# Optimization experiments

Hardware: AMD Instinct MI355X
Metric: run time of the kernel (lower is better)

## Reference

```python
import jax, jax.numpy as jnp
import numpy as np

MASK_VALUE = 0.0
LEAKY_SLOPE = 0.2  # tf.keras 'leaky_relu' activation default negative_slope

B, T, F, H, OUT = 256, 512, 256, 1024, 64


def setup_inputs() -> dict:
    key = jax.random.key(0)
    ks = jax.random.split(key, 5)
    x = jax.random.normal(ks[0], (B, T, F), dtype=jnp.float32)
    W = jax.random.normal(ks[1], (F, 4 * H), dtype=jnp.float32) * 0.05
    U = jax.random.normal(ks[2], (H, 4 * H), dtype=jnp.float32) * 0.05
    b = jnp.zeros((4 * H,), dtype=jnp.float32)
    W1 = jax.random.normal(ks[3], (3 * H, H), dtype=jnp.float32) * 0.02
    b1 = jnp.zeros((H,), dtype=jnp.float32)
    W2 = jax.random.normal(ks[4], (H, OUT), dtype=jnp.float32) * 0.02
    b2 = jnp.zeros((OUT,), dtype=jnp.float32)
    return {"x": x, "W": W, "U": U, "b": b, "W1": W1, "b1": b1, "W2": W2, "b2": b2}


def _lstm_final_state(x, mask, W, U, b):
    """Masked LSTM (Keras gate order i,f,g,o); masked steps carry state through.
    Returns final (h, c), each [B, H]. Dropout layers are identity at inference."""
    h0 = jnp.zeros((x.shape[0], H), dtype=x.dtype)
    c0 = jnp.zeros((x.shape[0], H), dtype=x.dtype)
    # Precompute input projection for all timesteps in one big GEMM: [B,T,4H]
    xz = jnp.einsum('btf,fg->btg', x, W) + b

    def step(carry, inp):
        h, c = carry
        xz_t, m_t = inp  # [B,4H], [B]
        z = xz_t + h @ U
        i, f, g, o = jnp.split(z, 4, axis=-1)
        i = jax.nn.sigmoid(i)
        f = jax.nn.sigmoid(f)
        g = jnp.tanh(g)
        o = jax.nn.sigmoid(o)
        c_new = f * c + i * g
        h_new = o * jnp.tanh(c_new)
        m = m_t[:, None]
        h = jnp.where(m, h_new, h)
        c = jnp.where(m, c_new, c)
        return (h, c), None

    xs = (jnp.swapaxes(xz, 0, 1), jnp.swapaxes(mask, 0, 1))  # time-major
    (h, c), _ = jax.lax.scan(step, (h0, c0), xs)
    return h, c


def reference(x, W, U, b, W1, b1, W2, b2):
    mask = jnp.any(x != MASK_VALUE, axis=2)  # [B,T]
    h, c = _lstm_final_state(x, mask, W, U, b)
    # return_state=True with return_sequences=False -> (out, h, c), out == h
    feat = jnp.concatenate([h, h, c], axis=1)  # [B, 3H]
    y = jax.nn.leaky_relu(feat @ W1 + b1, negative_slope=LEAKY_SLOPE)
    return y @ W2 + b2
```

## Files before the change

### kernel.cpp

```cpp
#include <hip/hip_runtime.h>

#define Tt_ 512
#define Ff_ 256
#define Hh_ 1024

typedef unsigned short u16;
typedef unsigned long long u64;
typedef __attribute__((ext_vector_type(8))) short bf16x8;
typedef __attribute__((ext_vector_type(4))) float f32x4;
typedef __attribute__((ext_vector_type(2))) unsigned int u32x2;

#define MFMA(a, b, c) __builtin_amdgcn_mfma_f32_16x16x32_bf16(a, b, c, 0, 0, 0)

__device__ __forceinline__ float bf2f(u16 u){
  union { unsigned int i; float f; } v; v.i = ((unsigned int)u) << 16; return v.f;
}
__device__ __forceinline__ u16 f2bf(float f){
  union { float f; unsigned int i; } v; v.f = f;
  return (u16)((v.i + 0x7FFFu + ((v.i >> 16) & 1u)) >> 16);
}
__device__ __forceinline__ float sigm(float z){ return 1.0f / (1.0f + __expf(-z)); }
__device__ __forceinline__ float tanh_(float z){ return 1.0f - 2.0f / (__expf(2.0f * z) + 1.0f); }
__device__ __forceinline__ float getE(const void* p, size_t i, int isf32){
  return isf32 ? ((const float*)p)[i] : bf2f(((const u16*)p)[i]);
}

template<int SEL>
__device__ __forceinline__ float qb(float v, int lbase){
#if __has_builtin(__builtin_amdgcn_mov_dpp)
  int r = __builtin_amdgcn_mov_dpp(__builtin_bit_cast(int, v), SEL * 0x55, 0xF, 0xF, true);
  return __builtin_bit_cast(float, r);
#else
  return __shfl(v, lbase + SEL, 64);
#endif
}

__global__ void detect_dtype(const u16* __restrict__ p, int* __restrict__ flag){
  int tid = threadIdx.x;
  int plausible = 0;
  for (int i = tid; i < 4096; i += 256){
    u16 u = p[2 * i];
    int ex = (u >> 7) & 0xFF;
    plausible += (((u & 0x7FFF) == 0) || (ex >= 87 && ex <= 133)) ? 1 : 0;
  }
  __shared__ int red[256];
  red[tid] = plausible; __syncthreads();
  for (int s = 128; s > 0; s >>= 1){ if (tid < s) red[tid] += red[tid + s]; __syncthreads(); }
  if (tid == 0) *flag = (red[0] < (4096 * 3) / 5) ? 1 : 0;
}

__global__ void convert_x(const void* __restrict__ x, u16* __restrict__ xb, const int* __restrict__ flags){
  size_t i = ((size_t)blockIdx.x * 256 + threadIdx.x) * 8;
  if (flags[0]){
    const float* xf = (const float*)x + i;
    u16 o[8];
    #pragma unroll
    for (int j = 0; j < 8; ++j) o[j] = f2bf(xf[j]);
    *(bf16x8*)(xb + i) = *(const bf16x8*)o;
  } else {
    *(bf16x8*)(xb + i) = *(const bf16x8*)((const u16*)x + i);
  }
}

__global__ void pack_wu(const void* __restrict__ W, const void* __restrict__ U,
                        const int* __restrict__ flags, u16* __restrict__ WUp){
  int fW = flags[1], fU = flags[2];
  int u = blockIdx.x * 256 + threadIdx.x;
  int nt = u / 10240;
  int rem = u - nt * 10240;
  int kg = rem >> 6, c64 = rem & 63;
  int pc = nt * 64 + c64;
  int g = pc & 3;
  int gb = ((g & 1) << 1) | (g >> 1);
  int oc = gb * 1024 + (pc >> 2);
  u16* dst = WUp + (size_t)u * 8;
  #pragma unroll
  for (int j = 0; j < 8; ++j){
    int k = kg * 8 + j;
    float v = (k < 256) ? getE(W, (size_t)k * 4096 + oc, fW)
                        : getE(U, (size_t)(k - 256) * 4096 + oc, fU);
    dst[j] = f2bf(v);
  }
}

__global__ void pack_w1(const void* __restrict__ W1, const int* __restrict__ flags, u16* __restrict__ W1p){
  int f1 = flags[3];
  int u = blockIdx.x * 256 + threadIdx.x;
  int nt = u >> 14;
  int kg = (u >> 6) & 255, c64 = u & 63;
  int n = nt * 64 + c64;
  u16* dst = W1p + (size_t)u * 8;
  #pragma unroll
  for (int j = 0; j < 8; ++j){
    int k = kg * 8 + j;
    float a = (k < 1024) ? getE(W1, (size_t)k * 1024 + n, f1) : 0.0f;
    a += getE(W1, (size_t)(k + 1024) * 1024 + n, f1);
    dst[j] = f2bf(a);
  }
}

__global__ void pack_w2(const void* __restrict__ W2, const int* __restrict__ flags, u16* __restrict__ W2p){
  int f2 = flags[4];
  int u = blockIdx.x * 256 + threadIdx.x;
  int kg = u >> 6, c64 = u & 63;
  u16* dst = W2p + (size_t)u * 8;
  #pragma unroll
  for (int j = 0; j < 8; ++j) dst[j] = f2bf(getE(W2, (size_t)(kg * 8 + j) * 64 + c64, f2));
}

__global__ void pack_bias(const u16* __restrict__ b, float* __restrict__ br){
  int u = blockIdx.x * 256 + threadIdx.x;
  int g = u & 3;
  int gb = ((g & 1) << 1) | (g >> 1);
  br[u] = bf2f(b[gb * 1024 + (u >> 2)]);
}

__global__ void mask_kernel(const u16* __restrict__ xb, unsigned char* __restrict__ mkT){
  int w = threadIdx.x >> 6, lane = threadIdx.x & 63;
  int row = blockIdx.x * 4 + w;
  u32x2 v = *((const u32x2*)(xb + (size_t)row * 256) + lane);
  int nz = (((v.x & 0x7FFF7FFFu) | (v.y & 0x7FFF7FFFu)) != 0u);
  int a = __any(nz);
  if (lane == 0){
    int b = row >> 9, t = row & 511;
    mkT[(size_t)t * 256 + b] = (unsigned char)(a ? 1 : 0);
  }
}

__launch_bounds__(512, 1)
__global__ void lstm_step(const u16* __restrict__ x, const u16* __restrict__ WUp,
                          const float* __restrict__ br, const unsigned char* __restrict__ mkT,
                          u16* __restrict__ hb0, u16* __restrict__ hb1,
                          u16* __restrict__ cfin, unsigned int* bar){
  __shared__ u64 hsm[8192];
  __shared__ u16 hstg[1024];
  __shared__ u16 Bc[2][22528];
  const int tid = threadIdx.x, bid = blockIdx.x;
  const int lane = tid & 63, w = tid >> 6;
  const int quad = lane >> 4, l15 = lane & 15;
  const int g  = (bid >> 3) & 7;
  const int c  = (bid & 7) | ((bid >> 6) << 3);
  const int r0 = g * 32;
  const int tile = w >> 2;
  const int nt = c * 2 + tile;
  const int bc0 = (w & 3) * 16 + l15;
  const u16* Bb = WUp + (size_t)nt * 81920;
  const int pc0 = c * 128 + w * 16 + l15;
  const float bias0 = br[pc0];
  const int slot = lane & 3, lbase = lane & 60;
  const int jl0 = w * 4 + (l15 >> 2);
  const int rowE = quad * 4;
  const size_t xrowA = (size_t)(r0 + l15) * (Tt_ * Ff_);
  const size_t xrowB = xrowA + (size_t)16 * Tt_ * Ff_;
  const int swzA = (l15 & 7) << 4;
  char* hb = (char*)hsm;
  unsigned int* mybar = bar + (g << 5);
  const int hr   = tid >> 4;
  const int hc16 = tid & 15;
  const size_t hgoff = (size_t)(r0 + hr) * Hh_ + hc16 * 4;
  const int hldsb = hr * 2048;
  const int hswz = (hr & 7) << 4;
  const int hcb = hc16 * 8;

  for (int i = tid; i < 5632; i += 512){
    int tl = i / 2816, rem = i - tl * 2816;
    *(bf16x8*)&Bc[tl][rem * 8] =
      *(const bf16x8*)(WUp + (size_t)(c * 2 + tl) * 81920 + (size_t)rem * 8);
  }
  __syncthreads();

  f32x4 cst[2];
  { f32x4 z4 = {0.f, 0.f, 0.f, 0.f}; cst[0] = z4; cst[1] = z4; }

  f32x4 accx[2];
  { f32x4 i0 = {bias0, bias0, bias0, bias0}; accx[0] = i0; accx[1] = i0; }
  {
    const u16* xp = x;
    #pragma unroll
    for (int ks = 0; ks < 8; ++ks){
      int kq = ks * 32 + quad * 8;
      bf16x8 a0 = *(const bf16x8*)(xp + xrowA + kq);
      bf16x8 a1 = *(const bf16x8*)(xp + xrowB + kq);
      bf16x8 b0 = *(const bf16x8*)(&Bc[tile][ks * 2048 + quad * 512 + bc0 * 8]);
      accx[0] = MFMA(a0, b0, accx[0]);
      accx[1] = MFMA(a1, b0, accx[1]);
    }
  }

  for (int t = 0; t < Tt_; ++t){
    const u16* hin  = (t & 1) ? hb1 : hb0;
    u16*       hout = (t & 1) ? hb0 : hb1;

    u64 hA[8], hB[8];
    #pragma unroll
    for (int i = 0; i < 8; ++i)
      hA[i] = __hip_atomic_load((const u64*)(hin + hgoff + i * 64),
                                __ATOMIC_RELAXED, __HIP_MEMORY_SCOPE_AGENT);
    #pragma unroll
    for (int i = 0; i < 8; ++i)
      hB[i] = __hip_atomic_load((const u64*)(hin + hgoff + (i + 8) * 64),
                                __ATOMIC_RELAXED, __HIP_MEMORY_SCOPE_AGENT);

    unsigned int mka = *(const unsigned int*)(mkT + (size_t)t * 256 + r0 + rowE);
    unsigned int mkb = *(const unsigned int*)(mkT + (size_t)t * 256 + r0 + rowE + 16);

    f32x4 acc[2];
    acc[0] = accx[0]; acc[1] = accx[1];

    #pragma unroll
    for (int i = 0; i < 8; ++i)
      *(u64*)(hb + hldsb + ((i * 128 + hcb) ^ hswz)) = hA[i];
    __syncthreads();

    #pragma unroll
    for (int ks = 0; ks < 3; ++ks){
      int cb = ks * 64 + quad * 16;
      bf16x8 a0 = *(const bf16x8*)(hb + l15 * 2048 + (cb ^ swzA));
      bf16x8 a1 = *(const bf16x8*)(hb + (l15 + 16) * 2048 + (cb ^ swzA));
      bf16x8 b0 = *(const bf16x8*)(&Bc[tile][(ks + 8) * 2048 + quad * 512 + bc0 * 8]);
      acc[0] = MFMA(a0, b0, acc[0]);
      acc[1] = MFMA(a1, b0, acc[1]);
    }
    #pragma unroll
    for (int ks = 3; ks < 16; ++ks){
      int cb = ks * 64 + quad * 16;
      bf16x8 a0 = *(const bf16x8*)(hb + l15 * 2048 + (cb ^ swzA));
      bf16x8 a1 = *(const bf16x8*)(hb + (l15 + 16) * 2048 + (cb ^ swzA));
      bf16x8 b0 = *(const bf16x8*)(Bb + (size_t)((ks + 8) * 4 + quad) * 512 + bc0 * 8);
      acc[0] = MFMA(a0, b0, acc[0]);
      acc[1] = MFMA(a1, b0, acc[1]);
    }

    #pragma unroll
    for (int i = 0; i < 8; ++i)
      *(u64*)(hb + hldsb + (((i + 8) * 128 + hcb) ^ hswz)) = hB[i];
    __syncthreads();

    #pragma unroll
    for (int ks = 16; ks < 32; ++ks){
      int cb = ks * 64 + quad * 16;
      bf16x8 a0 = *(const bf16x8*)(hb + l15 * 2048 + (cb ^ swzA));
      bf16x8 a1 = *(const bf16x8*)(hb + (l15 + 16) * 2048 + (cb ^ swzA));
      bf16x8 b0 = *(const bf16x8*)(Bb + (size_t)((ks + 8) * 4 + quad) * 512 + bc0 * 8);
      acc[0] = MFMA(a0, b0, acc[0]);
      acc[1] = MFMA(a1, b0, acc[1]);
    }

    #pragma unroll
    for (int mf = 0; mf < 2; ++mf){
      unsigned int mk4 = mf ? mkb : mka;
      #pragma unroll
      for (int reg = 0; reg < 4; ++reg){
        float z = acc[mf][reg];
        float v = (slot == 1) ? tanh_(z) : sigm(z);
        float vi = qb<0>(v, lbase);
        float vg = qb<1>(v, lbase);
        float vf = qb<2>(v, lbase);
        float vo = qb<3>(v, lbase);
        float cv = cst[mf][reg];
        float cn = fmaf(vf, cv, vi * vg);
        float hn = vo * tanh_(cn);
        if (!((mk4 >> (8 * reg)) & 1u)){
          cn = cv;
          int rl = rowE + reg + mf * 16;
          int jh = c * 32 + jl0;
          hn = bf2f(*(const u16*)(hb + rl * 2048 + ((jh * 2) ^ ((rl & 7) << 4))));
        }
        cst[mf][reg] = cn;
        if (slot == 0){
          int rl = rowE + reg + mf * 16;
          hstg[rl * 32 + jl0] = f2bf(hn);
        }
      }
    }
    __syncthreads();

    if (tid < 256){
      u64 val = ((const u64*)hstg)[tid];
      __hip_atomic_store((u64*)(hout + (size_t)(r0 + (tid >> 3)) * Hh_ + c * 32 + (tid & 7) * 4),
                         val, __ATOMIC_RELAXED, __HIP_MEMORY_SCOPE_AGENT);
    }
    __syncthreads();

    if (t < Tt_ - 1){
      if (tid == 0)
        __hip_atomic_fetch_add(mybar, 1u, __ATOMIC_RELAXED, __HIP_MEMORY_SCOPE_AGENT);

      { f32x4 i0 = {bias0, bias0, bias0, bias0}; accx[0] = i0; accx[1] = i0; }
      {
        const u16* xp = x + (size_t)(t + 1) * Ff_;
        #pragma unroll
        for (int ks = 0; ks < 8; ++ks){
          int kq = ks * 32 + quad * 8;
          bf16x8 a0 = *(const bf16x8*)(xp + xrowA + kq);
          bf16x8 a1 = *(const bf16x8*)(xp + xrowB + kq);
          bf16x8 b0 = *(const bf16x8*)(&Bc[tile][ks * 2048 + quad * 512 + bc0 * 8]);
          accx[0] = MFMA(a0, b0, accx[0]);
          accx[1] = MFMA(a1, b0, accx[1]);
        }
      }

      if (tid == 0){
        const unsigned int target = (unsigned int)(t + 1) * 32u;
        while (__hip_atomic_load(mybar, __ATOMIC_RELAXED, __HIP_MEMORY_SCOPE_AGENT) < target)
          __builtin_amdgcn_s_sleep(1);
      }
      __syncthreads();
    }
  }

  #pragma unroll
  for (int mf = 0; mf < 2; ++mf)
    #pragma unroll
    for (int reg = 0; reg < 4; ++reg)
      if (slot == 0){
        int r = r0 + rowE + reg + mf * 16;
        cfin[(size_t)r * Hh_ + c * 32 + jl0] = f2bf(cst[mf][reg]);
      }
}

__launch_bounds__(256, 1)
__global__ void gemm_head(const u16* __restrict__ A1, const u16* __restrict__ A2,
                          int kSplit, int kSlices, const u16* __restrict__ Bp,
                          int Ntiles, const u16* __restrict__ bias, int act,
                          void* __restrict__ outp, int ldOut, int outF32){
  const int tid = threadIdx.x, bid = blockIdx.x;
  const int lane = tid & 63, w = tid >> 6;
  const int wm = w >> 1, wn = w & 1;
  const int quad = lane >> 4, l15 = lane & 15;
  const int mt = bid / Ntiles, nt = bid - mt * Ntiles;
  const int r0 = mt * 64 + wm * 32 + l15;
  const size_t arow0 = (size_t)r0 * 1024;
  const size_t arow1 = arow0 + (size_t)16 * 1024;
  const int bc0 = wn * 32 + l15;
  const u16* Bb = Bp + (size_t)nt * kSlices * 2048;
  f32x4 acc[2][2];
  { f32x4 z4 = {0.f, 0.f, 0.f, 0.f}; acc[0][0] = z4; acc[0][1] = z4; acc[1][0] = z4; acc[1][1] = z4; }
  #pragma unroll 4
  for (int ks = 0; ks < kSlices; ++ks){
    const u16* ap; int kq;
    if (ks < kSplit){ ap = A1; kq = ks * 32 + quad * 8; }
    else            { ap = A2; kq = (ks - kSplit) * 32 + quad * 8; }
    bf16x8 a0 = *(const bf16x8*)(ap + arow0 + kq);
    bf16x8 a1 = *(const bf16x8*)(ap + arow1 + kq);
    const u16* bp = Bb + (size_t)(ks * 4 + quad) * 512;
    bf16x8 b0 = *(const bf16x8*)(bp + bc0 * 8);
    bf16x8 b1 = *(const bf16x8*)(bp + bc0 * 8 + 128);
    acc[0][0] = MFMA(a0, b0, acc[0][0]);
    acc[0][1] = MFMA(a0, b1, acc[0][1]);
    acc[1][0] = MFMA(a1, b0, acc[1][0]);
    acc[1][1] = MFMA(a1, b1, acc[1][1]);
  }
  #pragma unroll
  for (int mf = 0; mf < 2; ++mf)
    #pragma unroll
    for (int nf = 0; nf < 2; ++nf){
      int cB = nt * 64 + bc0 + nf * 16;
      #pragma unroll
      for (int reg = 0; reg < 4; ++reg){
        int r = mt * 64 + wm * 32 + mf * 16 + quad * 4 + reg;
        float zv = acc[mf][nf][reg] + bf2f(bias[cB]);
        if (act) zv = (zv > 0.f) ? zv : 0.2f * zv;
        if (outF32) ((float*)outp)[(size_t)r * ldOut + cB] = zv;
        else        ((u16*)outp)[(size_t)r * ldOut + cB] = f2bf(zv);
      }
    }
}

extern "C" void kernel_launch(void* const* d_in, const int* in_sizes, int n_in,
                              void* d_out, int out_size, void* d_ws, size_t ws_size,
                              hipStream_t stream){
  const void* x  = d_in[0];
  const void* W  = d_in[1];
  const void* U  = d_in[2];
  const u16*  b  = (const u16*)d_in[3];
  const void* W1 = d_in[4];
  const u16*  b1 = (const u16*)d_in[5];
  const void* W2 = d_in[6];
  const u16*  b2 = (const u16*)d_in[7];
  char* ws = (char*)d_ws;
  size_t o = 0;
  u16* WUp = (u16*)(ws + o);            o += 10485760;
  u16* W1p = (u16*)(ws + o);            o += 4194304;
  u16* W2p = (u16*)(ws + o);            o += 131072;
  float* br = (float*)(ws + o);         o += 16384;
  unsigned char* mk = (unsigned char*)(ws + o); o += 131072;
  u16* hb0 = (u16*)(ws + o);            o += 524288;
  u16* hb1 = (u16*)(ws + o);            o += 524288;
  u16* cfin = (u16*)(ws + o);           o += 524288;
  u16* yb  = (u16*)(ws + o);            o += 524288;
  unsigned int* bar = (unsigned int*)(ws + o); o += 1024;
  int* flg = (int*)(ws + o);            o += 512;
  u16* xb  = (u16*)(ws + o);            o += 67108864;
  if (ws_size < o) return;

  hipMemsetAsync(hb0, 0, 524288, stream);
  hipMemsetAsync(bar, 0, 1024, stream);
  detect_dtype<<<1, 256, 0, stream>>>((const u16*)x,  flg + 0);
  detect_dtype<<<1, 256, 0, stream>>>((const u16*)W,  flg + 1);
  detect_dtype<<<1, 256, 0, stream>>>((const u16*)U,  flg + 2);
  detect_dtype<<<1, 256, 0, stream>>>((const u16*)W1, flg + 3);
  detect_dtype<<<1, 256, 0, stream>>>((const u16*)W2, flg + 4);
  convert_x<<<16384, 256, 0, stream>>>(x, xb, flg);
  pack_wu<<<2560, 256, 0, stream>>>(W, U, flg, WUp);
  pack_w1<<<1024, 256, 0, stream>>>(W1, flg, W1p);
  pack_w2<<<32, 256, 0, stream>>>(W2, flg, W2p);
  pack_bias<<<16, 256, 0, stream>>>(b, br);
  mask_kernel<<<32768, 256, 0, stream>>>(xb, mk);
  lstm_step<<<256, 512, 0, stream>>>(xb, WUp, br, mk, hb0, hb1, cfin, bar);
  gemm_head<<<64, 256, 0, stream>>>(hb0, cfin, 32, 64, W1p, 16, b1, 1, yb, 1024, 0);
  gemm_head<<<4, 256, 0, stream>>>(yb, yb, 32, 32, W2p, 1, b2, 0, d_out, 64, 1);
}
```

Baseline: 4.946 ms.

## Replace per-group atomic counter barrier with per-block step flags polled by all waves

```diff
diff --git a/kernel.cpp b/kernel.cpp
--- a/kernel.cpp
+++ b/kernel.cpp
@@ -131,7 +131,7 @@
 __global__ void lstm_step(const u16* __restrict__ x, const u16* __restrict__ WUp,
                           const float* __restrict__ br, const unsigned char* __restrict__ mkT,
                           u16* __restrict__ hb0, u16* __restrict__ hb1,
-                          u16* __restrict__ cfin, unsigned int* bar){
+                          u16* __restrict__ cfin, unsigned int* flg32){
   __shared__ u64 hsm[8192];
   __shared__ u16 hstg[1024];
   __shared__ u16 Bc[2][22528];
@@ -154,7 +154,9 @@
   const size_t xrowB = xrowA + (size_t)16 * Tt_ * Ff_;
   const int swzA = (l15 & 7) << 4;
   char* hb = (char*)hsm;
-  unsigned int* mybar = bar + (g << 5);
+  const unsigned int* fpA = flg32 + (((g << 5) + (lane & 15)) << 4);
+  const unsigned int* fpB = fpA + (16 << 4);
+  unsigned int* myflag = flg32 + (((g << 5) + c) << 4);
   const int hr   = tid >> 4;
   const int hc16 = tid & 15;
   const size_t hgoff = (size_t)(r0 + hr) * Hh_ + hc16 * 4;
@@ -190,12 +192,20 @@
   for (int t = 0; t < Tt_; ++t){
     const u16* hin  = (t & 1) ? hb1 : hb0;
     u16*       hout = (t & 1) ? hb0 : hb1;
-
+    const unsigned int tgt = (unsigned int)t;
+
+    while (__ballot(__hip_atomic_load(fpA, __ATOMIC_RELAXED, __HIP_MEMORY_SCOPE_AGENT) >= tgt)
+           != ~0ull){}
+    asm volatile("" ::: "memory");
     u64 hA[8], hB[8];
     #pragma unroll
     for (int i = 0; i < 8; ++i)
       hA[i] = __hip_atomic_load((const u64*)(hin + hgoff + i * 64),
                                 __ATOMIC_RELAXED, __HIP_MEMORY_SCOPE_AGENT);
+
+    while (__ballot(__hip_atomic_load(fpB, __ATOMIC_RELAXED, __HIP_MEMORY_SCOPE_AGENT) >= tgt)
+           != ~0ull){}
+    asm volatile("" ::: "memory");
     #pragma unroll
     for (int i = 0; i < 8; ++i)
       hB[i] = __hip_atomic_load((const u64*)(hin + hgoff + (i + 8) * 64),
@@ -282,30 +292,22 @@
     }
     __syncthreads();
 
+    if (tid == 0)
+      __hip_atomic_store(myflag, (unsigned int)(t + 1),
+                         __ATOMIC_RELAXED, __HIP_MEMORY_SCOPE_AGENT);
+
     if (t < Tt_ - 1){
-      if (tid == 0)
-        __hip_atomic_fetch_add(mybar, 1u, __ATOMIC_RELAXED, __HIP_MEMORY_SCOPE_AGENT);
-
       { f32x4 i0 = {bias0, bias0, bias0, bias0}; accx[0] = i0; accx[1] = i0; }
-      {
-        const u16* xp = x + (size_t)(t + 1) * Ff_;
-        #pragma unroll
-        for (int ks = 0; ks < 8; ++ks){
-          int kq = ks * 32 + quad * 8;
-          bf16x8 a0 = *(const bf16x8*)(xp + xrowA + kq);
-          bf16x8 a1 = *(const bf16x8*)(xp + xrowB + kq);
-          bf16x8 b0 = *(const bf16x8*)(&Bc[tile][ks * 2048 + quad * 512 + bc0 * 8]);
-          accx[0] = MFMA(a0, b0, accx[0]);
-          accx[1] = MFMA(a1, b0, accx[1]);
-        }
+      const u16* xp = x + (size_t)(t + 1) * Ff_;
+      #pragma unroll
+      for (int ks = 0; ks < 8; ++ks){
+        int kq = ks * 32 + quad * 8;
+        bf16x8 a0 = *(const bf16x8*)(xp + xrowA + kq);
+        bf16x8 a1 = *(const bf16x8*)(xp + xrowB + kq);
+        bf16x8 b0 = *(const bf16x8*)(&Bc[tile][ks * 2048 + quad * 512 + bc0 * 8]);
+        accx[0] = MFMA(a0, b0, accx[0]);
+        accx[1] = MFMA(a1, b0, accx[1]);
       }
-
-      if (tid == 0){
-        const unsigned int target = (unsigned int)(t + 1) * 32u;
-        while (__hip_atomic_load(mybar, __ATOMIC_RELAXED, __HIP_MEMORY_SCOPE_AGENT) < target)
-          __builtin_amdgcn_s_sleep(1);
-      }
-      __syncthreads();
     }
   }
 
@@ -389,13 +391,13 @@
   u16* hb1 = (u16*)(ws + o);            o += 524288;
   u16* cfin = (u16*)(ws + o);           o += 524288;
   u16* yb  = (u16*)(ws + o);            o += 524288;
-  unsigned int* bar = (unsigned int*)(ws + o); o += 1024;
+  unsigned int* flg32 = (unsigned int*)(ws + o); o += 16384;
   int* flg = (int*)(ws + o);            o += 512;
   u16* xb  = (u16*)(ws + o);            o += 67108864;
   if (ws_size < o) return;
 
   hipMemsetAsync(hb0, 0, 524288, stream);
-  hipMemsetAsync(bar, 0, 1024, stream);
+  hipMemsetAsync(flg32, 0, 16384, stream);
   detect_dtype<<<1, 256, 0, stream>>>((const u16*)x,  flg + 0);
   detect_dtype<<<1, 256, 0, stream>>>((const u16*)W,  flg + 1);
   detect_dtype<<<1, 256, 0, stream>>>((const u16*)U,  flg + 2);
@@ -407,7 +409,7 @@
   pack_w2<<<32, 256, 0, stream>>>(W2, flg, W2p);
   pack_bias<<<16, 256, 0, stream>>>(b, br);
   mask_kernel<<<32768, 256, 0, stream>>>(xb, mk);
-  lstm_step<<<256, 512, 0, stream>>>(xb, WUp, br, mk, hb0, hb1, cfin, bar);
+  lstm_step<<<256, 512, 0, stream>>>(xb, WUp, br, mk, hb0, hb1, cfin, flg32);
   gemm_head<<<64, 256, 0, stream>>>(hb0, cfin, 32, 64, W1p, 16, b1, 1, yb, 1024, 0);
   gemm_head<<<4, 256, 0, stream>>>(yb, yb, 32, 32, W2p, 1, b2, 0, d_out, 64, 1);
 }
```

Result: slower. 5.119 ms (+3.5%).

## Split LSTM step rows across 16 waves with 1024-thread blocks

Applied to the files above, without the earlier changes.

```diff
diff --git a/kernel.cpp b/kernel.cpp
--- a/kernel.cpp
+++ b/kernel.cpp
@@ -127,7 +127,7 @@
   }
 }
 
-__launch_bounds__(512, 1)
+__launch_bounds__(1024, 1)
 __global__ void lstm_step(const u16* __restrict__ x, const u16* __restrict__ WUp,
                           const float* __restrict__ br, const unsigned char* __restrict__ mkT,
                           u16* __restrict__ hb0, u16* __restrict__ hb1,
@@ -141,49 +141,45 @@
   const int g  = (bid >> 3) & 7;
   const int c  = (bid & 7) | ((bid >> 6) << 3);
   const int r0 = g * 32;
-  const int tile = w >> 2;
-  const int nt = c * 2 + tile;
-  const int bc0 = (w & 3) * 16 + l15;
-  const u16* Bb = WUp + (size_t)nt * 81920;
-  const int pc0 = c * 128 + w * 16 + l15;
+  const int rh = w & 1;
+  const int cs = w >> 1;
+  const int tile = cs >> 2;
+  const int bc0 = (cs & 3) * 16 + l15;
+  const u16* Bb = WUp + (size_t)(c * 2 + tile) * 81920;
+  const int pc0 = c * 128 + cs * 16 + l15;
   const float bias0 = br[pc0];
   const int slot = lane & 3, lbase = lane & 60;
-  const int jl0 = w * 4 + (l15 >> 2);
+  const int jl0 = cs * 4 + (l15 >> 2);
+  const int rowL = rh * 16;
   const int rowE = quad * 4;
-  const size_t xrowA = (size_t)(r0 + l15) * (Tt_ * Ff_);
-  const size_t xrowB = xrowA + (size_t)16 * Tt_ * Ff_;
+  const size_t xrow = (size_t)(r0 + rowL + l15) * (Tt_ * Ff_);
   const int swzA = (l15 & 7) << 4;
   char* hb = (char*)hsm;
   unsigned int* mybar = bar + (g << 5);
-  const int hr   = tid >> 4;
-  const int hc16 = tid & 15;
-  const size_t hgoff = (size_t)(r0 + hr) * Hh_ + hc16 * 4;
+  const int hr   = tid >> 5;
+  const int hc32 = tid & 31;
+  const size_t hgoff = (size_t)(r0 + hr) * Hh_ + hc32 * 4;
   const int hldsb = hr * 2048;
   const int hswz = (hr & 7) << 4;
-  const int hcb = hc16 * 8;
-
-  for (int i = tid; i < 5632; i += 512){
+  const int hcb = hc32 * 8;
+
+  for (int i = tid; i < 5632; i += 1024){
     int tl = i / 2816, rem = i - tl * 2816;
     *(bf16x8*)&Bc[tl][rem * 8] =
       *(const bf16x8*)(WUp + (size_t)(c * 2 + tl) * 81920 + (size_t)rem * 8);
   }
   __syncthreads();
 
-  f32x4 cst[2];
-  { f32x4 z4 = {0.f, 0.f, 0.f, 0.f}; cst[0] = z4; cst[1] = z4; }
-
-  f32x4 accx[2];
-  { f32x4 i0 = {bias0, bias0, bias0, bias0}; accx[0] = i0; accx[1] = i0; }
+  f32x4 cst = {0.f, 0.f, 0.f, 0.f};
+
+  f32x4 accx = {bias0, bias0, bias0, bias0};
   {
     const u16* xp = x;
     #pragma unroll
     for (int ks = 0; ks < 8; ++ks){
-      int kq = ks * 32 + quad * 8;
-      bf16x8 a0 = *(const bf16x8*)(xp + xrowA + kq);
-      bf16x8 a1 = *(const bf16x8*)(xp + xrowB + kq);
+      bf16x8 a0 = *(const bf16x8*)(xp + xrow + ks * 32 + quad * 8);
       bf16x8 b0 = *(const bf16x8*)(&Bc[tile][ks * 2048 + quad * 512 + bc0 * 8]);
-      accx[0] = MFMA(a0, b0, accx[0]);
-      accx[1] = MFMA(a1, b0, accx[1]);
+      accx = MFMA(a0, b0, accx);
     }
   }
 
@@ -191,86 +187,74 @@
     const u16* hin  = (t & 1) ? hb1 : hb0;
     u16*       hout = (t & 1) ? hb0 : hb1;
 
-    u64 hA[8], hB[8];
-    #pragma unroll
-    for (int i = 0; i < 8; ++i)
-      hA[i] = __hip_atomic_load((const u64*)(hin + hgoff + i * 64),
+    u64 hA[4], hB[4];
+    #pragma unroll
+    for (int i = 0; i < 4; ++i)
+      hA[i] = __hip_atomic_load((const u64*)(hin + hgoff + i * 128),
                                 __ATOMIC_RELAXED, __HIP_MEMORY_SCOPE_AGENT);
     #pragma unroll
-    for (int i = 0; i < 8; ++i)
-      hB[i] = __hip_atomic_load((const u64*)(hin + hgoff + (i + 8) * 64),
+    for (int i = 0; i < 4; ++i)
+      hB[i] = __hip_atomic_load((const u64*)(hin + hgoff + (i + 4) * 128),
                                 __ATOMIC_RELAXED, __HIP_MEMORY_SCOPE_AGENT);
 
-    unsigned int mka = *(const unsigned int*)(mkT + (size_t)t * 256 + r0 + rowE);
-    unsigned int mkb = *(const unsigned int*)(mkT + (size_t)t * 256 + r0 + rowE + 16);
-
-    f32x4 acc[2];
-    acc[0] = accx[0]; acc[1] = accx[1];
-
-    #pragma unroll
-    for (int i = 0; i < 8; ++i)
-      *(u64*)(hb + hldsb + ((i * 128 + hcb) ^ hswz)) = hA[i];
+    unsigned int mk4 = *(const unsigned int*)(mkT + (size_t)t * 256 + r0 + rowL + rowE);
+
+    f32x4 acc = accx;
+
+    #pragma unroll
+    for (int i = 0; i < 4; ++i)
+      *(u64*)(hb + hldsb + ((i * 256 + hcb) ^ hswz)) = hA[i];
     __syncthreads();
 
     #pragma unroll
     for (int ks = 0; ks < 3; ++ks){
       int cb = ks * 64 + quad * 16;
-      bf16x8 a0 = *(const bf16x8*)(hb + l15 * 2048 + (cb ^ swzA));
-      bf16x8 a1 = *(const bf16x8*)(hb + (l15 + 16) * 2048 + (cb ^ swzA));
+      bf16x8 a0 = *(const bf16x8*)(hb + (rowL + l15) * 2048 + (cb ^ swzA));
       bf16x8 b0 = *(const bf16x8*)(&Bc[tile][(ks + 8) * 2048 + quad * 512 + bc0 * 8]);
-      acc[0] = MFMA(a0, b0, acc[0]);
-      acc[1] = MFMA(a1, b0, acc[1]);
+      acc = MFMA(a0, b0, acc);
     }
     #pragma unroll
     for (int ks = 3; ks < 16; ++ks){
       int cb = ks * 64 + quad * 16;
-      bf16x8 a0 = *(const bf16x8*)(hb + l15 * 2048 + (cb ^ swzA));
-      bf16x8 a1 = *(const bf16x8*)(hb + (l15 + 16) * 2048 + (cb ^ swzA));
+      bf16x8 a0 = *(const bf16x8*)(hb + (rowL + l15) * 2048 + (cb ^ swzA));
       bf16x8 b0 = *(const bf16x8*)(Bb + (size_t)((ks + 8) * 4 + quad) * 512 + bc0 * 8);
-      acc[0] = MFMA(a0, b0, acc[0]);
-      acc[1] = MFMA(a1, b0, acc[1]);
-    }
-
-    #pragma unroll
-    for (int i = 0; i < 8; ++i)
-      *(u64*)(hb + hldsb + (((i + 8) * 128 + hcb) ^ hswz)) = hB[i];
+      acc = MFMA(a0, b0, acc);
+    }
+
+    #pragma unroll
+    for (int i = 0; i < 4; ++i)
+      *(u64*)(hb + hldsb + (((i + 4) * 256 + hcb) ^ hswz)) = hB[i];
     __syncthreads();
 
     #pragma unroll
     for (int ks = 16; ks < 32; ++ks){
       int cb = ks * 64 + quad * 16;
-      bf16x8 a0 = *(const bf16x8*)(hb + l15 * 2048 + (cb ^ swzA));
-      bf16x8 a1 = *(const bf16x8*)(hb + (l15 + 16) * 2048 + (cb ^ swzA));
+      bf16x8 a0 = *(const bf16x8*)(hb + (rowL + l15) * 2048 + (cb ^ swzA));
       bf16x8 b0 = *(const bf16x8*)(Bb + (size_t)((ks + 8) * 4 + quad) * 512 + bc0 * 8);
-      acc[0] = MFMA(a0, b0, acc[0]);
-      acc[1] = MFMA(a1, b0, acc[1]);
-    }
-
-    #pragma unroll
-    for (int mf = 0; mf < 2; ++mf){
-      unsigned int mk4 = mf ? mkb : mka;
-      #pragma unroll
-      for (int reg = 0; reg < 4; ++reg){
-        float z = acc[mf][reg];
-        float v = (slot == 1) ? tanh_(z) : sigm(z);
-        float vi = qb<0>(v, lbase);
-        float vg = qb<1>(v, lbase);
-        float vf = qb<2>(v, lbase);
-        float vo = qb<3>(v, lbase);
-        float cv = cst[mf][reg];
-        float cn = fmaf(vf, cv, vi * vg);
-        float hn = vo * tanh_(cn);
-        if (!((mk4 >> (8 * reg)) & 1u)){
-          cn = cv;
-          int rl = rowE + reg + mf * 16;
-          int jh = c * 32 + jl0;
-          hn = bf2f(*(const u16*)(hb + rl * 2048 + ((jh * 2) ^ ((rl & 7) << 4))));
-        }
-        cst[mf][reg] = cn;
-        if (slot == 0){
-          int rl = rowE + reg + mf * 16;
-          hstg[rl * 32 + jl0] = f2bf(hn);
-        }
+      acc = MFMA(a0, b0, acc);
+    }
+
+    #pragma unroll
+    for (int reg = 0; reg < 4; ++reg){
+      float z = acc[reg];
+      float v = (slot == 1) ? tanh_(z) : sigm(z);
+      float vi = qb<0>(v, lbase);
+      float vg = qb<1>(v, lbase);
+      float vf = qb<2>(v, lbase);
+      float vo = qb<3>(v, lbase);
+      float cv = cst[reg];
+      float cn = fmaf(vf, cv, vi * vg);
+      float hn = vo * tanh_(cn);
+      if (!((mk4 >> (8 * reg)) & 1u)){
+        cn = cv;
+        int rl = rowL + rowE + reg;
+        int jh = c * 32 + jl0;
+        hn = bf2f(*(const u16*)(hb + rl * 2048 + ((jh * 2) ^ ((rl & 7) << 4))));
+      }
+      cst[reg] = cn;
+      if (slot == 0){
+        int rl = rowL + rowE + reg;
+        hstg[rl * 32 + jl0] = f2bf(hn);
       }
     }
     __syncthreads();
@@ -286,17 +270,14 @@
       if (tid == 0)
         __hip_atomic_fetch_add(mybar, 1u, __ATOMIC_RELAXED, __HIP_MEMORY_SCOPE_AGENT);
 
-      { f32x4 i0 = {bias0, bias0, bias0, bias0}; accx[0] = i0; accx[1] = i0; }
+      accx = (f32x4){bias0, bias0, bias0, bias0};
       {
         const u16* xp = x + (size_t)(t + 1) * Ff_;
         #pragma unroll
         for (int ks = 0; ks < 8; ++ks){
-          int kq = ks * 32 + quad * 8;
-          bf16x8 a0 = *(const bf16x8*)(xp + xrowA + kq);
-          bf16x8 a1 = *(const bf16x8*)(xp + xrowB + kq);
+          bf16x8 a0 = *(const bf16x8*)(xp + xrow + ks * 32 + quad * 8);
           bf16x8 b0 = *(const bf16x8*)(&Bc[tile][ks * 2048 + quad * 512 + bc0 * 8]);
-          accx[0] = MFMA(a0, b0, accx[0]);
-          accx[1] = MFMA(a1, b0, accx[1]);
+          accx = MFMA(a0, b0, accx);
         }
       }
 
@@ -310,13 +291,11 @@
   }
 
   #pragma unroll
-  for (int mf = 0; mf < 2; ++mf)
-    #pragma unroll
-    for (int reg = 0; reg < 4; ++reg)
-      if (slot == 0){
-        int r = r0 + rowE + reg + mf * 16;
-        cfin[(size_t)r * Hh_ + c * 32 + jl0] = f2bf(cst[mf][reg]);
-      }
+  for (int reg = 0; reg < 4; ++reg)
+    if (slot == 0){
+      int r = r0 + rowL + rowE + reg;
+      cfin[(size_t)r * Hh_ + c * 32 + jl0] = f2bf(cst[reg]);
+    }
 }
 
 __launch_bounds__(256, 1)
@@ -407,7 +386,7 @@
   pack_w2<<<32, 256, 0, stream>>>(W2, flg, W2p);
   pack_bias<<<16, 256, 0, stream>>>(b, br);
   mask_kernel<<<32768, 256, 0, stream>>>(xb, mk);
-  lstm_step<<<256, 512, 0, stream>>>(xb, WUp, br, mk, hb0, hb1, cfin, bar);
+  lstm_step<<<256, 1024, 0, stream>>>(xb, WUp, br, mk, hb0, hb1, cfin, bar);
   gemm_head<<<64, 256, 0, stream>>>(hb0, cfin, 32, 64, W1p, 16, b1, 1, yb, 1024, 0);
   gemm_head<<<4, 256, 0, stream>>>(yb, yb, 32, 32, W2p, 1, b2, 0, d_out, 64, 1);
 }
```

New measurement: 11.37 ms. 2.3x slower.
